# Optimization experiments

Measured on AMD Instinct MI355X. Metric: run time of the kernel, lower is better.

Reference implementation:

```python
import jax, jax.numpy as jnp
import numpy as np

N = 50000      # nodes
E = 800000     # edges
IN = 128       # in_channels
HID = 32       # hidden_channels (per head)
HEADS = 4
OUT = 128      # out_channels
NEG_SLOPE = 0.2  # PyG GATConv leaky relu slope


def setup_inputs() -> dict:
    key = jax.random.key(0)
    ks = jax.random.split(key, 10)
    x = jax.random.normal(ks[0], (N, IN), dtype=jnp.float32)
    edge_index = jax.random.randint(ks[1], (2, E), 0, N, dtype=jnp.int32)
    s1 = 1.0 / np.sqrt(IN)
    s2 = 1.0 / np.sqrt(HEADS * HID)
    W1 = jax.random.normal(ks[2], (IN, HEADS * HID), dtype=jnp.float32) * s1
    a_src1 = jax.random.normal(ks[3], (HEADS, HID), dtype=jnp.float32) * s1
    a_dst1 = jax.random.normal(ks[4], (HEADS, HID), dtype=jnp.float32) * s1
    b1 = jnp.zeros((HEADS * HID,), dtype=jnp.float32)
    W2 = jax.random.normal(ks[5], (HEADS * HID, OUT), dtype=jnp.float32) * s2
    a_src2 = jax.random.normal(ks[6], (1, OUT), dtype=jnp.float32) * s2
    a_dst2 = jax.random.normal(ks[7], (1, OUT), dtype=jnp.float32) * s2
    b2 = jnp.zeros((OUT,), dtype=jnp.float32)
    return {"x": x, "edge_index": edge_index, "W1": W1, "a_src1": a_src1,
            "a_dst1": a_dst1, "b1": b1, "W2": W2, "a_src2": a_src2,
            "a_dst2": a_dst2, "b2": b2}


def _gat_layer(x, src, dst, W, a_src, a_dst, bias, heads, out_c, concat, n):
    # dense projection then reshape to [N, H, C]
    h = (x @ W).reshape(n, heads, out_c)
    # per-node attention halves: [N, H]
    alpha_src = jnp.einsum('nhc,hc->nh', h, a_src)
    alpha_dst = jnp.einsum('nhc,hc->nh', h, a_dst)
    # per-edge logits, leaky relu (slope 0.2 as in PyG)
    logits = jax.nn.leaky_relu(alpha_src[src] + alpha_dst[dst], NEG_SLOPE)  # [E', H]
    # segment softmax over incoming edges of each destination node
    m = jax.ops.segment_max(logits, dst, num_segments=n)          # [N, H]
    e = jnp.exp(logits - m[dst])                                   # [E', H]
    denom = jax.ops.segment_sum(e, dst, num_segments=n)           # [N, H]
    alpha = e / (denom[dst] + 1e-16)                               # [E', H]
    # weighted scatter-aggregate of source features
    out = jax.ops.segment_sum(alpha[:, :, None] * h[src], dst, num_segments=n)  # [N, H, C]
    if concat:
        out = out.reshape(n, heads * out_c)
    else:
        out = out.mean(axis=1)
    return out + bias


def reference(x, edge_index, W1, a_src1, a_dst1, b1, W2, a_src2, a_dst2, b2):
    n = x.shape[0]
    # PyG GATConv adds self-loops by default
    loop = jnp.arange(n, dtype=edge_index.dtype)
    src = jnp.concatenate([edge_index[0], loop])
    dst = jnp.concatenate([edge_index[1], loop])
    h = _gat_layer(x, src, dst, W1, a_src1, a_dst1, b1, HEADS, HID, True, n)
    h = jax.nn.elu(h)
    # dropout is identity in eval mode
    out = _gat_layer(h, src, dst, W2, a_src2, a_dst2, b2, 1, OUT, False, n)
    return jax.nn.elu(out)
```

## Files before the change

### kernel.cpp

```cpp
#include <hip/hip_runtime.h>
#include <hip/hip_bf16.h>


typedef _Float16 half2_t __attribute__((ext_vector_type(2)));
typedef _Float16 half4_t __attribute__((ext_vector_type(4)));
typedef _Float16 f16x8 __attribute__((ext_vector_type(8)));
typedef float f32x4 __attribute__((ext_vector_type(4)));

#define NBLK1 128
#define SORT_CAP 6144

static __device__ __forceinline__ float leaky02(float x) {
    return x > 0.f ? x : 0.2f * x;
}
static __device__ __forceinline__ float elu1(float x) {
    return x > 0.f ? x : __expf(x) - 1.f;
}


__global__ __launch_bounds__(256) void prep_kernel(
    const int* __restrict__ dst, int* __restrict__ g_cnt, int E, int chunk,
    const float* __restrict__ W1, const float* __restrict__ W2,
    _Float16* __restrict__ Wt1, _Float16* __restrict__ Wt2, int nbkt) {
    int b = blockIdx.x;
    int t = threadIdx.x;
    if (b < NBLK1) {
        __shared__ int h[256];
        h[t] = 0;
        __syncthreads();
        int lo = b * chunk, hi = min(E, lo + chunk);
        for (int i = lo + t; i < hi; i += 256) atomicAdd(&h[dst[i] >> 8], 1);
        __syncthreads();
        if (t < nbkt) g_cnt[t * NBLK1 + b] = h[t];
    } else {
        int idx = (b - NBLK1) * 256 + t;
        int which = idx >> 14;
        int r = idx & 16383;
        int nc = r >> 7, k = r & 127;
        if (which == 0)
            Wt1[(size_t)nc * 128 + k] = (_Float16)W1[(size_t)k * 128 + nc];
        else
            Wt2[(size_t)nc * 128 + k] = (_Float16)W2[(size_t)k * 128 + nc];
    }
}

__global__ void scan_tile_kernel(const int* __restrict__ in, int* __restrict__ out,
                                 int* __restrict__ sums, int n) {
    __shared__ int sdata[256];
    int t = threadIdx.x;
    int base = blockIdx.x * 2048 + t * 8;
    int v[8];
    int run = 0;
#pragma unroll
    for (int i = 0; i < 8; ++i) {
        int idx = base + i;
        int x = (idx < n) ? in[idx] : 0;
        run += x;
        v[i] = run;
    }
    sdata[t] = run;
    __syncthreads();
    for (int off = 1; off < 256; off <<= 1) {
        int u = (t >= off) ? sdata[t - off] : 0;
        __syncthreads();
        sdata[t] += u;
        __syncthreads();
    }
    int excl = sdata[t] - run;
#pragma unroll
    for (int i = 0; i < 8; ++i) {
        int idx = base + i;
        if (idx < n) out[idx] = v[i] + excl;
    }
    if (t == 0) sums[blockIdx.x] = sdata[255];
}

__global__ void scan_sums_kernel(int* __restrict__ sums, int nb) {
    int t = threadIdx.x;
    int orig = (t < nb) ? sums[t] : 0;
    int v = orig;
#pragma unroll
    for (int off = 1; off < 64; off <<= 1) {
        int u = __shfl_up(v, off, 64);
        if (t >= off) v += u;
    }
    if (t < nb) sums[t] = v - orig;
}

__global__ void offs_kernel(const int* __restrict__ incl, const int* __restrict__ sums,
                            int* __restrict__ offs, int ncnt) {
    int i = blockIdx.x * blockDim.x + threadIdx.x;
    if (i <= ncnt) offs[i] = (i == 0) ? 0 : incl[i - 1] + sums[(i - 1) >> 11];
}


__global__ __launch_bounds__(256) void gemm1_fused_kernel(
    const float* __restrict__ X, const _Float16* __restrict__ Wt,
    _Float16* __restrict__ H16, int nrows, const int* __restrict__ src,
    const int* __restrict__ dst, const int* __restrict__ offs,
    int2* __restrict__ binned, int E, int chunk, int nGemm, int nbkt) {
    int b = blockIdx.x;
    int t = threadIdx.x;
    if (b < nGemm) {
        int wave = t >> 6, lane = t & 63;
        int m = lane & 15, q = lane >> 4;
        int arow = b * 64 + wave * 16 + m;
        bool rowok = arow < nrows;
        const float* xr = X + (size_t)arow * 128;
        f16x8 afrag[4];
#pragma unroll
        for (int s = 0; s < 4; ++s) {
            float4 v0 = make_float4(0.f, 0.f, 0.f, 0.f);
            float4 v1 = make_float4(0.f, 0.f, 0.f, 0.f);
            if (rowok) {
                v0 = *(const float4*)(xr + s * 32 + q * 8);
                v1 = *(const float4*)(xr + s * 32 + q * 8 + 4);
            }
            f16x8 a;
            a[0] = (_Float16)v0.x; a[1] = (_Float16)v0.y;
            a[2] = (_Float16)v0.z; a[3] = (_Float16)v0.w;
            a[4] = (_Float16)v1.x; a[5] = (_Float16)v1.y;
            a[6] = (_Float16)v1.z; a[7] = (_Float16)v1.w;
            afrag[s] = a;
        }
#pragma unroll
        for (int c = 0; c < 8; ++c) {
            f32x4 acc = {0.f, 0.f, 0.f, 0.f};
#pragma unroll
            for (int s = 0; s < 4; ++s) {
                f16x8 bfrag = *(const f16x8*)(Wt + (size_t)(c * 16 + m) * 128 + s * 32 + q * 8);
                acc = __builtin_amdgcn_mfma_f32_16x16x32_f16(afrag[s], bfrag, acc, 0, 0, 0);
            }
#pragma unroll
            for (int r = 0; r < 4; ++r) {
                int orow = b * 64 + wave * 16 + q * 4 + r;
                if (orow < nrows)
                    H16[(size_t)orow * 128 + c * 16 + m] = (_Float16)acc[r];
            }
        }
    } else {
        __shared__ int cur[256];
        int sb = b - nGemm;
        if (t < nbkt) cur[t] = offs[t * NBLK1 + sb];
        __syncthreads();
        int lo = sb * chunk, hi = min(E, lo + chunk);
        for (int i = lo + t; i < hi; i += 256) {
            int d = dst[i];
            int s = src[i];
            int p = atomicAdd(&cur[d >> 8], 1);
            binned[p] = make_int2(s, d);
        }
    }
}


__global__ __launch_bounds__(256) void sort_alpha1_kernel(
    const int2* __restrict__ binned, const int* __restrict__ offs,
    int* __restrict__ row_ptr, int* __restrict__ csr, int n, int nbkt,
    const _Float16* __restrict__ H16, const float* __restrict__ a_src,
    const float* __restrict__ a_dst, float* __restrict__ asrc_out,
    float* __restrict__ adst_out) {
    int b = blockIdx.x;
    int t = threadIdx.x;
    if (b < nbkt) {
        __shared__ int sorted[SORT_CAP];
        __shared__ int sdata[256];
        __shared__ int cur[256];
        int estart = offs[b * NBLK1];
        int eend = offs[(b + 1) * NBLK1];
        int node0 = b * 256;
        int nloc = min(256, n - node0);
        int cnt0 = (t < nloc) ? 1 : 0;
        cur[t] = cnt0;
        __syncthreads();
        for (int i = estart + t; i < eend; i += 256)
            atomicAdd(&cur[binned[i].y & 255], 1);
        __syncthreads();
        int my = cur[t];
        sdata[t] = my;
        __syncthreads();
        for (int off = 1; off < 256; off <<= 1) {
            int u = (t >= off) ? sdata[t - off] : 0;
            __syncthreads();
            sdata[t] += u;
            __syncthreads();
        }
        int excl = sdata[t] - my;
        int total = sdata[255];
        int csr_base = estart + node0;
        if (node0 + t <= n) row_ptr[node0 + t] = csr_base + excl;
        if (t == 0 && node0 + 256 <= n) row_ptr[node0 + 256] = csr_base + total;
        if (t < nloc) {
            if (excl < SORT_CAP) sorted[excl] = node0 + t;
            else csr[csr_base + excl] = node0 + t;
            cur[t] = excl + 1;
        } else {
            cur[t] = 0;
        }
        __syncthreads();
        for (int i = estart + t; i < eend; i += 256) {
            int2 pr = binned[i];
            int p = atomicAdd(&cur[pr.y & 255], 1);
            if (p < SORT_CAP) sorted[p] = pr.x;
            else csr[csr_base + p] = pr.x;
        }
        __syncthreads();
        int lim = min(total, SORT_CAP);
        for (int j = t; j < lim; j += 256) csr[csr_base + j] = sorted[j];
    } else {
        int node = (b - nbkt) * 4 + (t >> 6);
        int lane = t & 63;
        if (node >= n) return;
        int c = lane * 2;
        half2_t hv = *(const half2_t*)(H16 + (size_t)node * 128 + c);
        float2 as = *(const float2*)(a_src + c);
        float2 ad = *(const float2*)(a_dst + c);
        float hx = (float)hv.x, hy = (float)hv.y;
        float ps = hx * as.x + hy * as.y;
        float pd = hx * ad.x + hy * ad.y;
#pragma unroll
        for (int off = 1; off <= 8; off <<= 1) {
            ps += __shfl_xor(ps, off, 64);
            pd += __shfl_xor(pd, off, 64);
        }
        if ((lane & 15) == 0) {
            int h = lane >> 4;
            asrc_out[node * 4 + h] = ps;
            adst_out[node * 4 + h] = pd;
        }
    }
}

__global__ __launch_bounds__(256) void gemm2_mfma_kernel(
    const _Float16* __restrict__ A16, const _Float16* __restrict__ Wt,
    _Float16* __restrict__ H16, int nrows) {
    int b = blockIdx.x;
    int t = threadIdx.x;
    int wave = t >> 6, lane = t & 63;
    int m = lane & 15, q = lane >> 4;
    int arow = b * 64 + wave * 16 + m;
    bool rowok = arow < nrows;
    const _Float16* ar = A16 + (size_t)arow * 128;
    f16x8 afrag[4];
#pragma unroll
    for (int s = 0; s < 4; ++s) {
        f16x8 a = {};
        if (rowok) a = *(const f16x8*)(ar + s * 32 + q * 8);
        afrag[s] = a;
    }
#pragma unroll
    for (int c = 0; c < 8; ++c) {
        f32x4 acc = {0.f, 0.f, 0.f, 0.f};
#pragma unroll
        for (int s = 0; s < 4; ++s) {
            f16x8 bfrag = *(const f16x8*)(Wt + (size_t)(c * 16 + m) * 128 + s * 32 + q * 8);
            acc = __builtin_amdgcn_mfma_f32_16x16x32_f16(afrag[s], bfrag, acc, 0, 0, 0);
        }
#pragma unroll
        for (int r = 0; r < 4; ++r) {
            int orow = b * 64 + wave * 16 + q * 4 + r;
            if (orow < nrows)
                H16[(size_t)orow * 128 + c * 16 + m] = (_Float16)acc[r];
        }
    }
}

__global__ void alpha2_kernel(const _Float16* __restrict__ H16, const float* __restrict__ a_src,
                              const float* __restrict__ a_dst, float* __restrict__ asrc_out,
                              float* __restrict__ adst_out, int n) {
    int wave = (blockIdx.x * blockDim.x + threadIdx.x) >> 6;
    int lane = threadIdx.x & 63;
    if (wave >= n) return;
    int c = lane * 2;
    half2_t hv = *(const half2_t*)(H16 + (size_t)wave * 128 + c);
    float2 as = *(const float2*)(a_src + c);
    float2 ad = *(const float2*)(a_dst + c);
    float hx = (float)hv.x, hy = (float)hv.y;
    float ps = hx * as.x + hy * as.y;
    float pd = hx * ad.x + hy * ad.y;
#pragma unroll
    for (int off = 1; off <= 32; off <<= 1) {
        ps += __shfl_xor(ps, off, 64);
        pd += __shfl_xor(pd, off, 64);
    }
    if (lane == 0) {
        asrc_out[wave] = ps;
        adst_out[wave] = pd;
    }
}


__global__ __launch_bounds__(256) void agg1_kernel(
    const _Float16* __restrict__ H16, const float* __restrict__ asrc,
    const float* __restrict__ adst, const int* __restrict__ row_ptr,
    const int* __restrict__ csr, const float* __restrict__ bias,
    _Float16* __restrict__ out16, int n) {
    int wid = (blockIdx.x * blockDim.x + threadIdx.x) >> 6;
    int lane = threadIdx.x & 63;
    int node = wid * 2 + (lane >> 5);
    if (node >= n) return;
    int sub = lane & 31;
    int c = sub * 4;
    int h = sub >> 3;
    float adh = adst[node * 4 + h];
    float4 bv = *(const float4*)(bias + c);
    int e0 = row_ptr[node];
    int e1 = row_ptr[node + 1];
    float den = 0.f, a0 = 0.f, a1 = 0.f, a2 = 0.f, a3 = 0.f;
    int e = e0;
    for (; e + 8 <= e1; e += 8) {
        int s[8];
#pragma unroll
        for (int j = 0; j < 8; ++j) s[j] = csr[e + j];
        float l[8];
        half4_t g[8];
#pragma unroll
        for (int j = 0; j < 8; ++j) {
            l[j] = asrc[s[j] * 4 + h];
            g[j] = *(const half4_t*)(H16 + (size_t)s[j] * 128 + c);
        }
#pragma unroll
        for (int j = 0; j < 8; ++j) {
            float w = __expf(leaky02(l[j] + adh));
            den += w;
            a0 += w * (float)g[j].x;
            a1 += w * (float)g[j].y;
            a2 += w * (float)g[j].z;
            a3 += w * (float)g[j].w;
        }
    }
    for (; e + 4 <= e1; e += 4) {
        int s0 = csr[e + 0], s1 = csr[e + 1], s2 = csr[e + 2], s3 = csr[e + 3];
        float l0 = asrc[s0 * 4 + h], l1 = asrc[s1 * 4 + h];
        float l2 = asrc[s2 * 4 + h], l3 = asrc[s3 * 4 + h];
        half4_t g0 = *(const half4_t*)(H16 + (size_t)s0 * 128 + c);
        half4_t g1 = *(const half4_t*)(H16 + (size_t)s1 * 128 + c);
        half4_t g2 = *(const half4_t*)(H16 + (size_t)s2 * 128 + c);
        half4_t g3 = *(const half4_t*)(H16 + (size_t)s3 * 128 + c);
        float w0 = __expf(leaky02(l0 + adh));
        float w1 = __expf(leaky02(l1 + adh));
        float w2 = __expf(leaky02(l2 + adh));
        float w3 = __expf(leaky02(l3 + adh));
        den += (w0 + w1) + (w2 + w3);
        a0 += w0 * (float)g0.x + w1 * (float)g1.x + w2 * (float)g2.x + w3 * (float)g3.x;
        a1 += w0 * (float)g0.y + w1 * (float)g1.y + w2 * (float)g2.y + w3 * (float)g3.y;
        a2 += w0 * (float)g0.z + w1 * (float)g1.z + w2 * (float)g2.z + w3 * (float)g3.z;
        a3 += w0 * (float)g0.w + w1 * (float)g1.w + w2 * (float)g2.w + w3 * (float)g3.w;
    }
    for (; e < e1; ++e) {
        int s = csr[e];
        float w = __expf(leaky02(asrc[s * 4 + h] + adh));
        half4_t g = *(const half4_t*)(H16 + (size_t)s * 128 + c);
        den += w;
        a0 += w * (float)g.x;
        a1 += w * (float)g.y;
        a2 += w * (float)g.z;
        a3 += w * (float)g.w;
    }
    float inv = 1.f / (den + 1e-16f);
    half4_t o;
    o.x = (_Float16)elu1(a0 * inv + bv.x);
    o.y = (_Float16)elu1(a1 * inv + bv.y);
    o.z = (_Float16)elu1(a2 * inv + bv.z);
    o.w = (_Float16)elu1(a3 * inv + bv.w);
    *(half4_t*)(out16 + (size_t)node * 128 + c) = o;
}

__global__ __launch_bounds__(256) void agg2_kernel(
    const _Float16* __restrict__ H16, const float* __restrict__ asrc,
    const float* __restrict__ adst, const int* __restrict__ row_ptr,
    const int* __restrict__ csr, const float* __restrict__ bias,
    float* __restrict__ out, int n) {
    int wid = (blockIdx.x * blockDim.x + threadIdx.x) >> 6;
    int lane = threadIdx.x & 63;
    int node = wid * 2 + (lane >> 5);
    if (node >= n) return;
    int sub = lane & 31;
    int c = sub * 4;
    float adh = adst[node];
    float4 bv = *(const float4*)(bias + c);
    int e0 = row_ptr[node];
    int e1 = row_ptr[node + 1];
    float den = 0.f, a0 = 0.f, a1 = 0.f, a2 = 0.f, a3 = 0.f;
    int e = e0;
    for (; e + 8 <= e1; e += 8) {
        int s[8];
#pragma unroll
        for (int j = 0; j < 8; ++j) s[j] = csr[e + j];
        float l[8];
        half4_t g[8];
#pragma unroll
        for (int j = 0; j < 8; ++j) {
            l[j] = asrc[s[j]];
            g[j] = *(const half4_t*)(H16 + (size_t)s[j] * 128 + c);
        }
#pragma unroll
        for (int j = 0; j < 8; ++j) {
            float w = __expf(leaky02(l[j] + adh));
            den += w;
            a0 += w * (float)g[j].x;
            a1 += w * (float)g[j].y;
            a2 += w * (float)g[j].z;
            a3 += w * (float)g[j].w;
        }
    }
    for (; e + 4 <= e1; e += 4) {
        int s0 = csr[e + 0], s1 = csr[e + 1], s2 = csr[e + 2], s3 = csr[e + 3];
        float l0 = asrc[s0], l1 = asrc[s1], l2 = asrc[s2], l3 = asrc[s3];
        half4_t g0 = *(const half4_t*)(H16 + (size_t)s0 * 128 + c);
        half4_t g1 = *(const half4_t*)(H16 + (size_t)s1 * 128 + c);
        half4_t g2 = *(const half4_t*)(H16 + (size_t)s2 * 128 + c);
        half4_t g3 = *(const half4_t*)(H16 + (size_t)s3 * 128 + c);
        float w0 = __expf(leaky02(l0 + adh));
        float w1 = __expf(leaky02(l1 + adh));
        float w2 = __expf(leaky02(l2 + adh));
        float w3 = __expf(leaky02(l3 + adh));
        den += (w0 + w1) + (w2 + w3);
        a0 += w0 * (float)g0.x + w1 * (float)g1.x + w2 * (float)g2.x + w3 * (float)g3.x;
        a1 += w0 * (float)g0.y + w1 * (float)g1.y + w2 * (float)g2.y + w3 * (float)g3.y;
        a2 += w0 * (float)g0.z + w1 * (float)g1.z + w2 * (float)g2.z + w3 * (float)g3.z;
        a3 += w0 * (float)g0.w + w1 * (float)g1.w + w2 * (float)g2.w + w3 * (float)g3.w;
    }
    for (; e < e1; ++e) {
        int s = csr[e];
        float w = __expf(leaky02(asrc[s] + adh));
        half4_t g = *(const half4_t*)(H16 + (size_t)s * 128 + c);
        den += w;
        a0 += w * (float)g.x;
        a1 += w * (float)g.y;
        a2 += w * (float)g.z;
        a3 += w * (float)g.w;
    }
    float inv = 1.f / (den + 1e-16f);
    float4 o;
    o.x = elu1(a0 * inv + bv.x);
    o.y = elu1(a1 * inv + bv.y);
    o.z = elu1(a2 * inv + bv.z);
    o.w = elu1(a3 * inv + bv.w);
    *(float4*)(out + (size_t)node * 128 + c) = o;
}


extern "C" void kernel_launch(void* const* d_in, const int* in_sizes, int n_in,
                              void* d_out, int out_size, void* d_ws, size_t ws_size,
                              hipStream_t stream) {
    const float* x       = (const float*)d_in[0];
    const int*   eidx    = (const int*)d_in[1];
    const float* W1      = (const float*)d_in[2];
    const float* a_src1  = (const float*)d_in[3];
    const float* a_dst1  = (const float*)d_in[4];
    const float* b1      = (const float*)d_in[5];
    const float* W2      = (const float*)d_in[6];
    const float* a_src2  = (const float*)d_in[7];
    const float* a_dst2  = (const float*)d_in[8];
    const float* b2      = (const float*)d_in[9];
    float* out = (float*)d_out;

    const int N = in_sizes[0] / 128;
    const int E = in_sizes[1] / 2;
    const int* src = eidx;
    const int* dst = eidx + E;

    const int nbkt = (N + 255) >> 8;
    const int ncnt = nbkt * NBLK1;
    const int chunk = (E + NBLK1 - 1) / NBLK1;
    const int ntiles = (ncnt + 2047) / 2048;

    char* w = (char*)d_ws;
    _Float16* bufH16 = (_Float16*)w; w += (size_t)N * 128 * sizeof(_Float16);
    _Float16* Wt1    = (_Float16*)w; w += (size_t)128 * 128 * sizeof(_Float16);
    _Float16* Wt2    = (_Float16*)w; w += (size_t)128 * 128 * sizeof(_Float16);
    float* asrc = (float*)w;   w += (size_t)N * 4 * sizeof(float);
    float* adst = (float*)w;   w += (size_t)N * 4 * sizeof(float);
    int* g_cnt   = (int*)w;    w += (size_t)ncnt * sizeof(int);
    int* incl    = (int*)w;    w += (size_t)ncnt * sizeof(int);
    int* offs    = (int*)w;    w += (size_t)(ncnt + 1) * sizeof(int);
    int* sums    = (int*)w;    w += 64 * sizeof(int);
    int* row_ptr = (int*)w;    w += (size_t)(N + 1) * sizeof(int);
    int2* binned = (int2*)w;   w += (size_t)E * sizeof(int2);
    int* csr     = (int*)w;    w += (size_t)(E + N) * sizeof(int);
    _Float16* bufA16 = (_Float16*)d_out;

    dim3 b256(256);
    const int nGemm = (N + 63) / 64;
    const int nAlpha = (N + 3) / 4;
    dim3 gAgg(((((N + 1) / 2) + 3) / 4));

    hipLaunchKernelGGL(prep_kernel, dim3(NBLK1 + 128), b256, 0, stream, dst, g_cnt, E, chunk,
                       W1, W2, Wt1, Wt2, nbkt);
    hipLaunchKernelGGL(scan_tile_kernel, dim3(ntiles), b256, 0, stream, g_cnt, incl, sums, ncnt);
    hipLaunchKernelGGL(scan_sums_kernel, dim3(1), dim3(64), 0, stream, sums, ntiles);
    hipLaunchKernelGGL(offs_kernel, dim3((ncnt + 256) / 256 + 1), b256, 0, stream, incl, sums,
                       offs, ncnt);

    hipLaunchKernelGGL(gemm1_fused_kernel, dim3(nGemm + NBLK1), b256, 0, stream, x, Wt1,
                       bufH16, N, src, dst, offs, binned, E, chunk, nGemm, nbkt);
    hipLaunchKernelGGL(sort_alpha1_kernel, dim3(nbkt + nAlpha), b256, 0, stream, binned, offs,
                       row_ptr, csr, N, nbkt, bufH16, a_src1, a_dst1, asrc, adst);
    hipLaunchKernelGGL(agg1_kernel, gAgg, b256, 0, stream, bufH16, asrc, adst, row_ptr, csr, b1,
                       bufA16, N);

    hipLaunchKernelGGL(gemm2_mfma_kernel, dim3(nGemm), b256, 0, stream, bufA16, Wt2, bufH16, N);
    hipLaunchKernelGGL(alpha2_kernel, dim3(nAlpha), b256, 0, stream, bufH16, a_src2, a_dst2,
                       asrc, adst, N);
    hipLaunchKernelGGL(agg2_kernel, gAgg, b256, 0, stream, bufH16, asrc, adst, row_ptr, csr, b2,
                       out, N);
}
```

Measured before the change: 247.3 us.

## Fuse attention logits into GEMM epilogues, single-block scan, 16-bit CSR indices

The attention-half dot products (alpha_src/alpha_dst) are now computed inside both MFMA GEMM epilogues with shuffle reductions, which removes the separate alpha kernels and their re-read of H. The three-kernel scan is replaced by one single-block kernel. Binned edges are packed into one int, and CSR source indices are stored as unsigned short, cutting index traffic in the sort and aggregation kernels. The 16-bit packing assumes fewer than 65536 nodes, and the single-block scan serializes a small amount of work.

Measured after the change: 267.6 us. 1.08x slower.

```diff
diff --git a/kernel.cpp b/kernel.cpp
--- a/kernel.cpp
+++ b/kernel.cpp
@@ -44,61 +44,39 @@
     }
 }
 
-__global__ void scan_tile_kernel(const int* __restrict__ in, int* __restrict__ out,
-                                 int* __restrict__ sums, int n) {
-    __shared__ int sdata[256];
+
+__global__ __launch_bounds__(256) void scan_one_kernel(const int* __restrict__ g_cnt,
+                                                       int* __restrict__ offs, int ncnt) {
+    __shared__ int ssum[256];
     int t = threadIdx.x;
-    int base = blockIdx.x * 2048 + t * 8;
-    int v[8];
-    int run = 0;
-#pragma unroll
-    for (int i = 0; i < 8; ++i) {
-        int idx = base + i;
-        int x = (idx < n) ? in[idx] : 0;
-        run += x;
-        v[i] = run;
-    }
-    sdata[t] = run;
+    int per = (ncnt + 255) / 256;
+    int lo = t * per, hi = min(ncnt, lo + per);
+    int s = 0;
+    for (int i = lo; i < hi; ++i) s += g_cnt[i];
+    ssum[t] = s;
     __syncthreads();
     for (int off = 1; off < 256; off <<= 1) {
-        int u = (t >= off) ? sdata[t - off] : 0;
-        __syncthreads();
-        sdata[t] += u;
-        __syncthreads();
-    }
-    int excl = sdata[t] - run;
-#pragma unroll
-    for (int i = 0; i < 8; ++i) {
-        int idx = base + i;
-        if (idx < n) out[idx] = v[i] + excl;
-    }
-    if (t == 0) sums[blockIdx.x] = sdata[255];
-}
-
-__global__ void scan_sums_kernel(int* __restrict__ sums, int nb) {
-    int t = threadIdx.x;
-    int orig = (t < nb) ? sums[t] : 0;
-    int v = orig;
-#pragma unroll
-    for (int off = 1; off < 64; off <<= 1) {
-        int u = __shfl_up(v, off, 64);
-        if (t >= off) v += u;
-    }
-    if (t < nb) sums[t] = v - orig;
-}
-
-__global__ void offs_kernel(const int* __restrict__ incl, const int* __restrict__ sums,
-                            int* __restrict__ offs, int ncnt) {
-    int i = blockIdx.x * blockDim.x + threadIdx.x;
-    if (i <= ncnt) offs[i] = (i == 0) ? 0 : incl[i - 1] + sums[(i - 1) >> 11];
+        int u = (t >= off) ? ssum[t - off] : 0;
+        __syncthreads();
+        ssum[t] += u;
+        __syncthreads();
+    }
+    int run = ssum[t] - s;
+    for (int i = lo; i < hi; ++i) {
+        offs[i] = run;
+        run += g_cnt[i];
+    }
+    if (t == 255) offs[ncnt] = run;
 }
 
 
 __global__ __launch_bounds__(256) void gemm1_fused_kernel(
     const float* __restrict__ X, const _Float16* __restrict__ Wt,
-    _Float16* __restrict__ H16, int nrows, const int* __restrict__ src,
+    _Float16* __restrict__ H16, int nrows, const float* __restrict__ a_src,
+    const float* __restrict__ a_dst, float* __restrict__ asrc_out,
+    float* __restrict__ adst_out, const int* __restrict__ src,
     const int* __restrict__ dst, const int* __restrict__ offs,
-    int2* __restrict__ binned, int E, int chunk, int nGemm, int nbkt) {
+    int* __restrict__ binned, int E, int chunk, int nGemm, int nbkt) {
     int b = blockIdx.x;
     int t = threadIdx.x;
     if (b < nGemm) {
@@ -123,6 +101,11 @@
             a[6] = (_Float16)v1.z; a[7] = (_Float16)v1.w;
             afrag[s] = a;
         }
+        float ps[4][4], pd[4][4];
+#pragma unroll
+        for (int r = 0; r < 4; ++r)
+#pragma unroll
+            for (int hh = 0; hh < 4; ++hh) { ps[r][hh] = 0.f; pd[r][hh] = 0.f; }
 #pragma unroll
         for (int c = 0; c < 8; ++c) {
             f32x4 acc = {0.f, 0.f, 0.f, 0.f};
@@ -131,11 +114,40 @@
                 f16x8 bfrag = *(const f16x8*)(Wt + (size_t)(c * 16 + m) * 128 + s * 32 + q * 8);
                 acc = __builtin_amdgcn_mfma_f32_16x16x32_f16(afrag[s], bfrag, acc, 0, 0, 0);
             }
+            float asv = a_src[c * 16 + m];
+            float adv = a_dst[c * 16 + m];
 #pragma unroll
             for (int r = 0; r < 4; ++r) {
+                ps[r][c >> 1] += acc[r] * asv;
+                pd[r][c >> 1] += acc[r] * adv;
                 int orow = b * 64 + wave * 16 + q * 4 + r;
                 if (orow < nrows)
                     H16[(size_t)orow * 128 + c * 16 + m] = (_Float16)acc[r];
+            }
+        }
+#pragma unroll
+        for (int r = 0; r < 4; ++r)
+#pragma unroll
+            for (int hh = 0; hh < 4; ++hh) {
+                float v = ps[r][hh], u = pd[r][hh];
+#pragma unroll
+                for (int off = 1; off <= 8; off <<= 1) {
+                    v += __shfl_xor(v, off, 64);
+                    u += __shfl_xor(u, off, 64);
+                }
+                ps[r][hh] = v; pd[r][hh] = u;
+            }
+        if (m == 0) {
+#pragma unroll
+            for (int r = 0; r < 4; ++r) {
+                int row = b * 64 + wave * 16 + q * 4 + r;
+                if (row < nrows) {
+#pragma unroll
+                    for (int hh = 0; hh < 4; ++hh) {
+                        asrc_out[row * 4 + hh] = ps[r][hh];
+                        adst_out[row * 4 + hh] = pd[r][hh];
+                    }
+                }
             }
         }
     } else {
@@ -148,92 +160,69 @@
             int d = dst[i];
             int s = src[i];
             int p = atomicAdd(&cur[d >> 8], 1);
-            binned[p] = make_int2(s, d);
-        }
-    }
-}
-
-
-__global__ __launch_bounds__(256) void sort_alpha1_kernel(
-    const int2* __restrict__ binned, const int* __restrict__ offs,
-    int* __restrict__ row_ptr, int* __restrict__ csr, int n, int nbkt,
-    const _Float16* __restrict__ H16, const float* __restrict__ a_src,
+            binned[p] = ((d & 255) << 16) | s;
+        }
+    }
+}
+
+
+__global__ __launch_bounds__(256) void sort_kernel(
+    const int* __restrict__ binned, const int* __restrict__ offs,
+    int* __restrict__ row_ptr, unsigned short* __restrict__ csr, int n, int nbkt) {
+    __shared__ int sorted[SORT_CAP];
+    __shared__ int sdata[256];
+    __shared__ int cur[256];
+    int b = blockIdx.x;
+    int t = threadIdx.x;
+    int estart = offs[b * NBLK1];
+    int eend = offs[(b + 1) * NBLK1];
+    int node0 = b * 256;
+    int nloc = min(256, n - node0);
+    cur[t] = (t < nloc) ? 1 : 0;
+    __syncthreads();
+    for (int i = estart + t; i < eend; i += 256)
+        atomicAdd(&cur[(binned[i] >> 16) & 255], 1);
+    __syncthreads();
+    int my = cur[t];
+    sdata[t] = my;
+    __syncthreads();
+    for (int off = 1; off < 256; off <<= 1) {
+        int u = (t >= off) ? sdata[t - off] : 0;
+        __syncthreads();
+        sdata[t] += u;
+        __syncthreads();
+    }
+    int excl = sdata[t] - my;
+    int total = sdata[255];
+    int csr_base = estart + node0;
+    if (node0 + t <= n) row_ptr[node0 + t] = csr_base + excl;
+    if (t == 0 && node0 + 256 <= n) row_ptr[node0 + 256] = csr_base + total;
+    if (t < nloc) {
+        if (excl < SORT_CAP) sorted[excl] = node0 + t;
+        else csr[csr_base + excl] = (unsigned short)(node0 + t);
+        cur[t] = excl + 1;
+    } else {
+        cur[t] = 0;
+    }
+    __syncthreads();
+    for (int i = estart + t; i < eend; i += 256) {
+        int v = binned[i];
+        int p = atomicAdd(&cur[(v >> 16) & 255], 1);
+        int sv = v & 0xffff;
+        if (p < SORT_CAP) sorted[p] = sv;
+        else csr[csr_base + p] = (unsigned short)sv;
+    }
+    __syncthreads();
+    int lim = min(total, SORT_CAP);
+    for (int j = t; j < lim; j += 256) csr[csr_base + j] = (unsigned short)sorted[j];
+}
+
+
+__global__ __launch_bounds__(256) void gemm2_fused_kernel(
+    const _Float16* __restrict__ A16, const _Float16* __restrict__ Wt,
+    _Float16* __restrict__ H16, int nrows, const float* __restrict__ a_src,
     const float* __restrict__ a_dst, float* __restrict__ asrc_out,
     float* __restrict__ adst_out) {
-    int b = blockIdx.x;
-    int t = threadIdx.x;
-    if (b < nbkt) {
-        __shared__ int sorted[SORT_CAP];
-        __shared__ int sdata[256];
-        __shared__ int cur[256];
-        int estart = offs[b * NBLK1];
-        int eend = offs[(b + 1) * NBLK1];
-        int node0 = b * 256;
-        int nloc = min(256, n - node0);
-        int cnt0 = (t < nloc) ? 1 : 0;
-        cur[t] = cnt0;
-        __syncthreads();
-        for (int i = estart + t; i < eend; i += 256)
-            atomicAdd(&cur[binned[i].y & 255], 1);
-        __syncthreads();
-        int my = cur[t];
-        sdata[t] = my;
-        __syncthreads();
-        for (int off = 1; off < 256; off <<= 1) {
-            int u = (t >= off) ? sdata[t - off] : 0;
-            __syncthreads();
-            sdata[t] += u;
-            __syncthreads();
-        }
-        int excl = sdata[t] - my;
-        int total = sdata[255];
-        int csr_base = estart + node0;
-        if (node0 + t <= n) row_ptr[node0 + t] = csr_base + excl;
-        if (t == 0 && node0 + 256 <= n) row_ptr[node0 + 256] = csr_base + total;
-        if (t < nloc) {
-            if (excl < SORT_CAP) sorted[excl] = node0 + t;
-            else csr[csr_base + excl] = node0 + t;
-            cur[t] = excl + 1;
-        } else {
-            cur[t] = 0;
-        }
-        __syncthreads();
-        for (int i = estart + t; i < eend; i += 256) {
-            int2 pr = binned[i];
-            int p = atomicAdd(&cur[pr.y & 255], 1);
-            if (p < SORT_CAP) sorted[p] = pr.x;
-            else csr[csr_base + p] = pr.x;
-        }
-        __syncthreads();
-        int lim = min(total, SORT_CAP);
-        for (int j = t; j < lim; j += 256) csr[csr_base + j] = sorted[j];
-    } else {
-        int node = (b - nbkt) * 4 + (t >> 6);
-        int lane = t & 63;
-        if (node >= n) return;
-        int c = lane * 2;
-        half2_t hv = *(const half2_t*)(H16 + (size_t)node * 128 + c);
-        float2 as = *(const float2*)(a_src + c);
-        float2 ad = *(const float2*)(a_dst + c);
-        float hx = (float)hv.x, hy = (float)hv.y;
-        float ps = hx * as.x + hy * as.y;
-        float pd = hx * ad.x + hy * ad.y;
-#pragma unroll
-        for (int off = 1; off <= 8; off <<= 1) {
-            ps += __shfl_xor(ps, off, 64);
-            pd += __shfl_xor(pd, off, 64);
-        }
-        if ((lane & 15) == 0) {
-            int h = lane >> 4;
-            asrc_out[node * 4 + h] = ps;
-            adst_out[node * 4 + h] = pd;
-        }
-    }
-}
-
-__global__ __launch_bounds__(256) void gemm2_mfma_kernel(
-    const _Float16* __restrict__ A16, const _Float16* __restrict__ Wt,
-    _Float16* __restrict__ H16, int nrows) {
     int b = blockIdx.x;
     int t = threadIdx.x;
     int wave = t >> 6, lane = t & 63;
@@ -248,6 +237,8 @@
         if (rowok) a = *(const f16x8*)(ar + s * 32 + q * 8);
         afrag[s] = a;
     }
+    float ps[4] = {0.f, 0.f, 0.f, 0.f};
+    float pd[4] = {0.f, 0.f, 0.f, 0.f};
 #pragma unroll
     for (int c = 0; c < 8; ++c) {
         f32x4 acc = {0.f, 0.f, 0.f, 0.f};
@@ -256,36 +247,36 @@
             f16x8 bfrag = *(const f16x8*)(Wt + (size_t)(c * 16 + m) * 128 + s * 32 + q * 8);
             acc = __builtin_amdgcn_mfma_f32_16x16x32_f16(afrag[s], bfrag, acc, 0, 0, 0);
         }
+        float asv = a_src[c * 16 + m];
+        float adv = a_dst[c * 16 + m];
 #pragma unroll
         for (int r = 0; r < 4; ++r) {
+            ps[r] += acc[r] * asv;
+            pd[r] += acc[r] * adv;
             int orow = b * 64 + wave * 16 + q * 4 + r;
             if (orow < nrows)
                 H16[(size_t)orow * 128 + c * 16 + m] = (_Float16)acc[r];
         }
     }
-}
-
-__global__ void alpha2_kernel(const _Float16* __restrict__ H16, const float* __restrict__ a_src,
-                              const float* __restrict__ a_dst, float* __restrict__ asrc_out,
-                              float* __restrict__ adst_out, int n) {
-    int wave = (blockIdx.x * blockDim.x + threadIdx.x) >> 6;
-    int lane = threadIdx.x & 63;
-    if (wave >= n) return;
-    int c = lane * 2;
-    half2_t hv = *(const half2_t*)(H16 + (size_t)wave * 128 + c);
-    float2 as = *(const float2*)(a_src + c);
-    float2 ad = *(const float2*)(a_dst + c);
-    float hx = (float)hv.x, hy = (float)hv.y;
-    float ps = hx * as.x + hy * as.y;
-    float pd = hx * ad.x + hy * ad.y;
-#pragma unroll
-    for (int off = 1; off <= 32; off <<= 1) {
-        ps += __shfl_xor(ps, off, 64);
-        pd += __shfl_xor(pd, off, 64);
-    }
-    if (lane == 0) {
-        asrc_out[wave] = ps;
-        adst_out[wave] = pd;
+#pragma unroll
+    for (int r = 0; r < 4; ++r) {
+        float v = ps[r], u = pd[r];
+#pragma unroll
+        for (int off = 1; off <= 8; off <<= 1) {
+            v += __shfl_xor(v, off, 64);
+            u += __shfl_xor(u, off, 64);
+        }
+        ps[r] = v; pd[r] = u;
+    }
+    if (m == 0) {
+#pragma unroll
+        for (int r = 0; r < 4; ++r) {
+            int row = b * 64 + wave * 16 + q * 4 + r;
+            if (row < nrows) {
+                asrc_out[row] = ps[r];
+                adst_out[row] = pd[r];
+            }
+        }
     }
 }
 
@@ -293,7 +284,7 @@
 __global__ __launch_bounds__(256) void agg1_kernel(
     const _Float16* __restrict__ H16, const float* __restrict__ asrc,
     const float* __restrict__ adst, const int* __restrict__ row_ptr,
-    const int* __restrict__ csr, const float* __restrict__ bias,
+    const unsigned short* __restrict__ csr, const float* __restrict__ bias,
     _Float16* __restrict__ out16, int n) {
     int wid = (blockIdx.x * blockDim.x + threadIdx.x) >> 6;
     int lane = threadIdx.x & 63;
@@ -369,7 +360,7 @@
 __global__ __launch_bounds__(256) void agg2_kernel(
     const _Float16* __restrict__ H16, const float* __restrict__ asrc,
     const float* __restrict__ adst, const int* __restrict__ row_ptr,
-    const int* __restrict__ csr, const float* __restrict__ bias,
+    const unsigned short* __restrict__ csr, const float* __restrict__ bias,
     float* __restrict__ out, int n) {
     int wid = (blockIdx.x * blockDim.x + threadIdx.x) >> 6;
     int lane = threadIdx.x & 63;
@@ -464,7 +455,6 @@
     const int nbkt = (N + 255) >> 8;
     const int ncnt = nbkt * NBLK1;
     const int chunk = (E + NBLK1 - 1) / NBLK1;
-    const int ntiles = (ncnt + 2047) / 2048;
 
     char* w = (char*)d_ws;
     _Float16* bufH16 = (_Float16*)w; w += (size_t)N * 128 * sizeof(_Float16);
@@ -473,36 +463,31 @@
     float* asrc = (float*)w;   w += (size_t)N * 4 * sizeof(float);
     float* adst = (float*)w;   w += (size_t)N * 4 * sizeof(float);
     int* g_cnt   = (int*)w;    w += (size_t)ncnt * sizeof(int);
-    int* incl    = (int*)w;    w += (size_t)ncnt * sizeof(int);
     int* offs    = (int*)w;    w += (size_t)(ncnt + 1) * sizeof(int);
-    int* sums    = (int*)w;    w += 64 * sizeof(int);
     int* row_ptr = (int*)w;    w += (size_t)(N + 1) * sizeof(int);
-    int2* binned = (int2*)w;   w += (size_t)E * sizeof(int2);
-    int* csr     = (int*)w;    w += (size_t)(E + N) * sizeof(int);
+    int* binned  = (int*)w;    w += (size_t)E * sizeof(int);
+    unsigned short* csr = (unsigned short*)w;
+    w += (((size_t)(E + N) * sizeof(unsigned short) + 3) & ~(size_t)3);
     _Float16* bufA16 = (_Float16*)d_out;
 
     dim3 b256(256);
     const int nGemm = (N + 63) / 64;
-    const int nAlpha = (N + 3) / 4;
     dim3 gAgg(((((N + 1) / 2) + 3) / 4));
 
     hipLaunchKernelGGL(prep_kernel, dim3(NBLK1 + 128), b256, 0, stream, dst, g_cnt, E, chunk,
                        W1, W2, Wt1, Wt2, nbkt);
-    hipLaunchKernelGGL(scan_tile_kernel, dim3(ntiles), b256, 0, stream, g_cnt, incl, sums, ncnt);
-    hipLaunchKernelGGL(scan_sums_kernel, dim3(1), dim3(64), 0, stream, sums, ntiles);
-    hipLaunchKernelGGL(offs_kernel, dim3((ncnt + 256) / 256 + 1), b256, 0, stream, incl, sums,
-                       offs, ncnt);
+    hipLaunchKernelGGL(scan_one_kernel, dim3(1), b256, 0, stream, g_cnt, offs, ncnt);
 
     hipLaunchKernelGGL(gemm1_fused_kernel, dim3(nGemm + NBLK1), b256, 0, stream, x, Wt1,
-                       bufH16, N, src, dst, offs, binned, E, chunk, nGemm, nbkt);
-    hipLaunchKernelGGL(sort_alpha1_kernel, dim3(nbkt + nAlpha), b256, 0, stream, binned, offs,
-                       row_ptr, csr, N, nbkt, bufH16, a_src1, a_dst1, asrc, adst);
+                       bufH16, N, a_src1, a_dst1, asrc, adst, src, dst, offs, binned, E, chunk,
+                       nGemm, nbkt);
+    hipLaunchKernelGGL(sort_kernel, dim3(nbkt), b256, 0, stream, binned, offs, row_ptr, csr,
+                       N, nbkt);
     hipLaunchKernelGGL(agg1_kernel, gAgg, b256, 0, stream, bufH16, asrc, adst, row_ptr, csr, b1,
                        bufA16, N);
 
-    hipLaunchKernelGGL(gemm2_mfma_kernel, dim3(nGemm), b256, 0, stream, bufA16, Wt2, bufH16, N);
-    hipLaunchKernelGGL(alpha2_kernel, dim3(nAlpha), b256, 0, stream, bufH16, a_src2, a_dst2,
-                       asrc, adst, N);
+    hipLaunchKernelGGL(gemm2_fused_kernel, dim3(nGemm), b256, 0, stream, bufA16, Wt2, bufH16, N,
+                       a_src2, a_dst2, asrc, adst);
     hipLaunchKernelGGL(agg2_kernel, gAgg, b256, 0, stream, bufH16, asrc, adst, row_ptr, csr, b2,
                        out, N);
 }
```

## Pack binned edges into one int and widen aggregation loads to 16 bytes

Applied to the files above, without the earlier changes.

The edge binning buffer now stores each edge as a single 32-bit word, holding the source index in the low 16 bits and the destination's local offset in the high bits, instead of an int2. This halves the binned traffic in both the scatter and the sort passes. The aggregation kernels now assign 16 lanes per node, each loading 8 fp16 channels at once, and drop the 4-edge middle loop. The packing assumes source indices fit in 16 bits, but N is 50000, so this holds only because N < 65536. Fewer lanes per node means more nodes per wave, at the cost of more registers per lane.

Measured after the change: 253.0 us. +2.3%, slower.

```diff
diff --git a/kernel.cpp b/kernel.cpp
--- a/kernel.cpp
+++ b/kernel.cpp
@@ -98,7 +98,7 @@
     const float* __restrict__ X, const _Float16* __restrict__ Wt,
     _Float16* __restrict__ H16, int nrows, const int* __restrict__ src,
     const int* __restrict__ dst, const int* __restrict__ offs,
-    int2* __restrict__ binned, int E, int chunk, int nGemm, int nbkt) {
+    int* __restrict__ binned, int E, int chunk, int nGemm, int nbkt) {
     int b = blockIdx.x;
     int t = threadIdx.x;
     if (b < nGemm) {
@@ -148,14 +148,14 @@
             int d = dst[i];
             int s = src[i];
             int p = atomicAdd(&cur[d >> 8], 1);
-            binned[p] = make_int2(s, d);
+            binned[p] = ((d & 255) << 16) | s;
         }
     }
 }
 
 
 __global__ __launch_bounds__(256) void sort_alpha1_kernel(
-    const int2* __restrict__ binned, const int* __restrict__ offs,
+    const int* __restrict__ binned, const int* __restrict__ offs,
     int* __restrict__ row_ptr, int* __restrict__ csr, int n, int nbkt,
     const _Float16* __restrict__ H16, const float* __restrict__ a_src,
     const float* __restrict__ a_dst, float* __restrict__ asrc_out,
@@ -170,11 +170,10 @@
         int eend = offs[(b + 1) * NBLK1];
         int node0 = b * 256;
         int nloc = min(256, n - node0);
-        int cnt0 = (t < nloc) ? 1 : 0;
-        cur[t] = cnt0;
+        cur[t] = (t < nloc) ? 1 : 0;
         __syncthreads();
         for (int i = estart + t; i < eend; i += 256)
-            atomicAdd(&cur[binned[i].y & 255], 1);
+            atomicAdd(&cur[(binned[i] >> 16) & 255], 1);
         __syncthreads();
         int my = cur[t];
         sdata[t] = my;
@@ -199,10 +198,11 @@
         }
         __syncthreads();
         for (int i = estart + t; i < eend; i += 256) {
-            int2 pr = binned[i];
-            int p = atomicAdd(&cur[pr.y & 255], 1);
-            if (p < SORT_CAP) sorted[p] = pr.x;
-            else csr[csr_base + p] = pr.x;
+            int v = binned[i];
+            int p = atomicAdd(&cur[(v >> 16) & 255], 1);
+            int sv = v & 0xffff;
+            if (p < SORT_CAP) sorted[p] = sv;
+            else csr[csr_base + p] = sv;
         }
         __syncthreads();
         int lim = min(total, SORT_CAP);
@@ -297,73 +297,59 @@
     _Float16* __restrict__ out16, int n) {
     int wid = (blockIdx.x * blockDim.x + threadIdx.x) >> 6;
     int lane = threadIdx.x & 63;
-    int node = wid * 2 + (lane >> 5);
+    int node = wid * 4 + (lane >> 4);
     if (node >= n) return;
-    int sub = lane & 31;
-    int c = sub * 4;
-    int h = sub >> 3;
+    int sub = lane & 15;
+    int c = sub * 8;
+    int h = sub >> 2;
     float adh = adst[node * 4 + h];
-    float4 bv = *(const float4*)(bias + c);
+    float4 bv0 = *(const float4*)(bias + c);
+    float4 bv1 = *(const float4*)(bias + c + 4);
     int e0 = row_ptr[node];
     int e1 = row_ptr[node + 1];
-    float den = 0.f, a0 = 0.f, a1 = 0.f, a2 = 0.f, a3 = 0.f;
+    float den = 0.f;
+    float a[8];
+#pragma unroll
+    for (int k = 0; k < 8; ++k) a[k] = 0.f;
     int e = e0;
     for (; e + 8 <= e1; e += 8) {
         int s[8];
 #pragma unroll
         for (int j = 0; j < 8; ++j) s[j] = csr[e + j];
         float l[8];
-        half4_t g[8];
+        f16x8 g[8];
 #pragma unroll
         for (int j = 0; j < 8; ++j) {
             l[j] = asrc[s[j] * 4 + h];
-            g[j] = *(const half4_t*)(H16 + (size_t)s[j] * 128 + c);
+            g[j] = *(const f16x8*)(H16 + (size_t)s[j] * 128 + c);
         }
 #pragma unroll
         for (int j = 0; j < 8; ++j) {
             float w = __expf(leaky02(l[j] + adh));
             den += w;
-            a0 += w * (float)g[j].x;
-            a1 += w * (float)g[j].y;
-            a2 += w * (float)g[j].z;
-            a3 += w * (float)g[j].w;
-        }
-    }
-    for (; e + 4 <= e1; e += 4) {
-        int s0 = csr[e + 0], s1 = csr[e + 1], s2 = csr[e + 2], s3 = csr[e + 3];
-        float l0 = asrc[s0 * 4 + h], l1 = asrc[s1 * 4 + h];
-        float l2 = asrc[s2 * 4 + h], l3 = asrc[s3 * 4 + h];
-        half4_t g0 = *(const half4_t*)(H16 + (size_t)s0 * 128 + c);
-        half4_t g1 = *(const half4_t*)(H16 + (size_t)s1 * 128 + c);
-        half4_t g2 = *(const half4_t*)(H16 + (size_t)s2 * 128 + c);
-        half4_t g3 = *(const half4_t*)(H16 + (size_t)s3 * 128 + c);
-        float w0 = __expf(leaky02(l0 + adh));
-        float w1 = __expf(leaky02(l1 + adh));
-        float w2 = __expf(leaky02(l2 + adh));
-        float w3 = __expf(leaky02(l3 + adh));
-        den += (w0 + w1) + (w2 + w3);
-        a0 += w0 * (float)g0.x + w1 * (float)g1.x + w2 * (float)g2.x + w3 * (float)g3.x;
-        a1 += w0 * (float)g0.y + w1 * (float)g1.y + w2 * (float)g2.y + w3 * (float)g3.y;
-        a2 += w0 * (float)g0.z + w1 * (float)g1.z + w2 * (float)g2.z + w3 * (float)g3.z;
-        a3 += w0 * (float)g0.w + w1 * (float)g1.w + w2 * (float)g2.w + w3 * (float)g3.w;
+#pragma unroll
+            for (int k = 0; k < 8; ++k) a[k] += w * (float)g[j][k];
+        }
     }
     for (; e < e1; ++e) {
         int s = csr[e];
         float w = __expf(leaky02(asrc[s * 4 + h] + adh));
-        half4_t g = *(const half4_t*)(H16 + (size_t)s * 128 + c);
+        f16x8 g = *(const f16x8*)(H16 + (size_t)s * 128 + c);
         den += w;
-        a0 += w * (float)g.x;
-        a1 += w * (float)g.y;
-        a2 += w * (float)g.z;
-        a3 += w * (float)g.w;
+#pragma unroll
+        for (int k = 0; k < 8; ++k) a[k] += w * (float)g[k];
     }
     float inv = 1.f / (den + 1e-16f);
-    half4_t o;
-    o.x = (_Float16)elu1(a0 * inv + bv.x);
-    o.y = (_Float16)elu1(a1 * inv + bv.y);
-    o.z = (_Float16)elu1(a2 * inv + bv.z);
-    o.w = (_Float16)elu1(a3 * inv + bv.w);
-    *(half4_t*)(out16 + (size_t)node * 128 + c) = o;
+    f16x8 o;
+    o[0] = (_Float16)elu1(a[0] * inv + bv0.x);
+    o[1] = (_Float16)elu1(a[1] * inv + bv0.y);
+    o[2] = (_Float16)elu1(a[2] * inv + bv0.z);
+    o[3] = (_Float16)elu1(a[3] * inv + bv0.w);
+    o[4] = (_Float16)elu1(a[4] * inv + bv1.x);
+    o[5] = (_Float16)elu1(a[5] * inv + bv1.y);
+    o[6] = (_Float16)elu1(a[6] * inv + bv1.z);
+    o[7] = (_Float16)elu1(a[7] * inv + bv1.w);
+    *(f16x8*)(out16 + (size_t)node * 128 + c) = o;
 }
 
 __global__ __launch_bounds__(256) void agg2_kernel(
@@ -373,71 +359,59 @@
     float* __restrict__ out, int n) {
     int wid = (blockIdx.x * blockDim.x + threadIdx.x) >> 6;
     int lane = threadIdx.x & 63;
-    int node = wid * 2 + (lane >> 5);
+    int node = wid * 4 + (lane >> 4);
     if (node >= n) return;
-    int sub = lane & 31;
-    int c = sub * 4;
+    int sub = lane & 15;
+    int c = sub * 8;
     float adh = adst[node];
-    float4 bv = *(const float4*)(bias + c);
+    float4 bv0 = *(const float4*)(bias + c);
+    float4 bv1 = *(const float4*)(bias + c + 4);
     int e0 = row_ptr[node];
     int e1 = row_ptr[node + 1];
-    float den = 0.f, a0 = 0.f, a1 = 0.f, a2 = 0.f, a3 = 0.f;
+    float den = 0.f;
+    float a[8];
+#pragma unroll
+    for (int k = 0; k < 8; ++k) a[k] = 0.f;
     int e = e0;
     for (; e + 8 <= e1; e += 8) {
         int s[8];
 #pragma unroll
         for (int j = 0; j < 8; ++j) s[j] = csr[e + j];
         float l[8];
-        half4_t g[8];
+        f16x8 g[8];
 #pragma unroll
         for (int j = 0; j < 8; ++j) {
             l[j] = asrc[s[j]];
-            g[j] = *(const half4_t*)(H16 + (size_t)s[j] * 128 + c);
+            g[j] = *(const f16x8*)(H16 + (size_t)s[j] * 128 + c);
         }
 #pragma unroll
         for (int j = 0; j < 8; ++j) {
             float w = __expf(leaky02(l[j] + adh));
             den += w;
-            a0 += w * (float)g[j].x;
-            a1 += w * (float)g[j].y;
-            a2 += w * (float)g[j].z;
-            a3 += w * (float)g[j].w;
-        }
-    }
-    for (; e + 4 <= e1; e += 4) {
-        int s0 = csr[e + 0], s1 = csr[e + 1], s2 = csr[e + 2], s3 = csr[e + 3];
-        float l0 = asrc[s0], l1 = asrc[s1], l2 = asrc[s2], l3 = asrc[s3];
-        half4_t g0 = *(const half4_t*)(H16 + (size_t)s0 * 128 + c);
-        half4_t g1 = *(const half4_t*)(H16 + (size_t)s1 * 128 + c);
-        half4_t g2 = *(const half4_t*)(H16 + (size_t)s2 * 128 + c);
-        half4_t g3 = *(const half4_t*)(H16 + (size_t)s3 * 128 + c);
-        float w0 = __expf(leaky02(l0 + adh));
-        float w1 = __expf(leaky02(l1 + adh));
-        float w2 = __expf(leaky02(l2 + adh));
-        float w3 = __expf(leaky02(l3 + adh));
-        den += (w0 + w1) + (w2 + w3);
-        a0 += w0 * (float)g0.x + w1 * (float)g1.x + w2 * (float)g2.x + w3 * (float)g3.x;
-        a1 += w0 * (float)g0.y + w1 * (float)g1.y + w2 * (float)g2.y + w3 * (float)g3.y;
-        a2 += w0 * (float)g0.z + w1 * (float)g1.z + w2 * (float)g2.z + w3 * (float)g3.z;
-        a3 += w0 * (float)g0.w + w1 * (float)g1.w + w2 * (float)g2.w + w3 * (float)g3.w;
+#pragma unroll
+            for (int k = 0; k < 8; ++k) a[k] += w * (float)g[j][k];
+        }
     }
     for (; e < e1; ++e) {
         int s = csr[e];
         float w = __expf(leaky02(asrc[s] + adh));
-        half4_t g = *(const half4_t*)(H16 + (size_t)s * 128 + c);
+        f16x8 g = *(const f16x8*)(H16 + (size_t)s * 128 + c);
         den += w;
-        a0 += w * (float)g.x;
-        a1 += w * (float)g.y;
-        a2 += w * (float)g.z;
-        a3 += w * (float)g.w;
+#pragma unroll
+        for (int k = 0; k < 8; ++k) a[k] += w * (float)g[k];
     }
     float inv = 1.f / (den + 1e-16f);
-    float4 o;
-    o.x = elu1(a0 * inv + bv.x);
-    o.y = elu1(a1 * inv + bv.y);
-    o.z = elu1(a2 * inv + bv.z);
-    o.w = elu1(a3 * inv + bv.w);
-    *(float4*)(out + (size_t)node * 128 + c) = o;
+    float4 o0, o1;
+    o0.x = elu1(a[0] * inv + bv0.x);
+    o0.y = elu1(a[1] * inv + bv0.y);
+    o0.z = elu1(a[2] * inv + bv0.z);
+    o0.w = elu1(a[3] * inv + bv0.w);
+    o1.x = elu1(a[4] * inv + bv1.x);
+    o1.y = elu1(a[5] * inv + bv1.y);
+    o1.z = elu1(a[6] * inv + bv1.z);
+    o1.w = elu1(a[7] * inv + bv1.w);
+    *(float4*)(out + (size_t)node * 128 + c) = o0;
+    *(float4*)(out + (size_t)node * 128 + c + 4) = o1;
 }
 
 
@@ -477,14 +451,14 @@
     int* offs    = (int*)w;    w += (size_t)(ncnt + 1) * sizeof(int);
     int* sums    = (int*)w;    w += 64 * sizeof(int);
     int* row_ptr = (int*)w;    w += (size_t)(N + 1) * sizeof(int);
-    int2* binned = (int2*)w;   w += (size_t)E * sizeof(int2);
+    int* binned  = (int*)w;    w += (size_t)E * sizeof(int);
     int* csr     = (int*)w;    w += (size_t)(E + N) * sizeof(int);
     _Float16* bufA16 = (_Float16*)d_out;
 
     dim3 b256(256);
     const int nGemm = (N + 63) / 64;
     const int nAlpha = (N + 3) / 4;
-    dim3 gAgg(((((N + 1) / 2) + 3) / 4));
+    dim3 gAgg((((N + 3) / 4) + 3) / 4);
 
     hipLaunchKernelGGL(prep_kernel, dim3(NBLK1 + 128), b256, 0, stream, dst, g_cnt, E, chunk,
                        W1, W2, Wt1, Wt2, nbkt);
```
